# Optimization experiments

Measured on AMD Instinct MI355X. Metric: run time of the kernel, lower is better.

The kernel has to match this reference:

```python
import jax, jax.numpy as jnp
import numpy as np

B, S, HQ, HKV, D = 2, 2048, 32, 8, 128
ROPE_BASE = 10000.0
NEG_INF = -1e9


def setup_inputs() -> dict:
    key = jax.random.key(0)
    kq, kk, kv = jax.random.split(key, 3)
    q = jax.random.normal(kq, (B, S, HQ, D), dtype=jnp.float32)
    k = jax.random.normal(kk, (B, S, HKV, D), dtype=jnp.float32)
    v = jax.random.normal(kv, (B, S, HKV, D), dtype=jnp.float32)
    # Llama rotary tables: [S, D] with freqs duplicated across the two halves
    inv_freq = 1.0 / (ROPE_BASE ** (jnp.arange(0, D, 2, dtype=jnp.float32) / D))
    freqs = jnp.arange(S, dtype=jnp.float32)[:, None] * inv_freq[None, :]  # [S, D/2]
    emb = jnp.concatenate([freqs, freqs], axis=-1)  # [S, D]
    cos = jnp.cos(emb)
    sin = jnp.sin(emb)
    # causal additive mask [B, 1, S, S]: 0 on/below diagonal, -1e9 above
    causal = jnp.tril(jnp.ones((S, S), dtype=bool))
    attention_mask = jnp.where(causal, 0.0, NEG_INF).astype(jnp.float32)
    attention_mask = jnp.broadcast_to(attention_mask[None, None], (B, 1, S, S))
    return {
        "query_states": q,
        "key_states": k,
        "value_states": v,
        "cos": cos,
        "sin": sin,
        "attention_mask": attention_mask,
        "softmax_scale": float(1.0 / np.sqrt(D)),
    }


def _rotate_half(x):
    h = x.shape[-1] // 2
    return jnp.concatenate([-x[..., h:], x[..., :h]], axis=-1)


def _apply_rope(x, cos, sin):
    # x: [B, S, H, D]; cos/sin: [S, D] -> broadcast over batch and heads
    c = cos[None, :, None, :]
    s = sin[None, :, None, :]
    return x * c + _rotate_half(x) * s


def reference(query_states, key_states, value_states, cos, sin, attention_mask, softmax_scale):
    if attention_mask.ndim == 4 and attention_mask.shape[1] == 1:
        attention_mask = attention_mask[:, 0]  # [B, S, S]
    q = _apply_rope(query_states, cos, sin)          # [B, S, HQ, D]
    k = _apply_rope(key_states, cos, sin)            # [B, S, HKV, D]
    v = value_states                                  # [B, S, HKV, D]
    groups = q.shape[2] // k.shape[2]
    k = jnp.repeat(k, groups, axis=2)                 # [B, S, HQ, D]
    v = jnp.repeat(v, groups, axis=2)
    scores = jnp.einsum("bqhd,bkhd->bhqk", q, k) * softmax_scale
    scores = scores + attention_mask[:, None, :, :]   # broadcast over heads
    probs = jax.nn.softmax(scores, axis=-1)
    out = jnp.einsum("bhqk,bkhd->bqhd", probs, v)     # [B, S, HQ, D]
    return out
```

## Files before the change

kernel.cpp:

```cpp
#include <hip/hip_runtime.h>
#include <stdint.h>

typedef unsigned short u16;
typedef unsigned int   u32;
typedef short bf16x8 __attribute__((ext_vector_type(8)));
typedef u16   u16x8  __attribute__((ext_vector_type(8)));
typedef u16   u16x4  __attribute__((ext_vector_type(4)));
typedef float f32x4  __attribute__((ext_vector_type(4)));

#define B_   2
#define S_   2048
#define HQ_  32
#define HKV_ 8
#define D_   128
#define SCALE 0.08838834764831845f

#define KR_ELEMS (B_*HKV_*S_*D_)

#define KT_BLOCKS ((B_*S_*HKV_*16) / 256)
#define VT_BLOCKS (B_*HKV_*(S_/64))

#define SWZ(x) ((x) ^ (((x) >> 3) & 0x70))

__device__ __forceinline__ float b2f(u16 x) { return __uint_as_float(((u32)x) << 16); }
__device__ __forceinline__ u16 f2b(float f) {
  u32 u = __float_as_uint(f);
  return (u16)((u + 0x7FFFu + ((u >> 16) & 1u)) >> 16);
}
__device__ __forceinline__ bool is_f32(const void* cs) {
  return ((const u32*)cs)[0] == 0x3F800000u;
}

__device__ __forceinline__ void gload16(const u16* g, u16* l) {
  __builtin_amdgcn_global_load_lds(
      (const __attribute__((address_space(1))) u32*)g,
      (__attribute__((address_space(3))) u32*)l, 16, 0, 0);
}

__global__ __launch_bounds__(256) void rope_pre(
    const void* __restrict__ kin, const void* __restrict__ vin,
    const void* __restrict__ cs, const void* __restrict__ sn, u16* __restrict__ ws)
{
  const bool f32 = is_f32(cs);
  const int bx = blockIdx.x;
  const int t  = threadIdx.x;
  __shared__ u16 tile[64 * 136];

  if (bx < KT_BLOCKS) {
    int tid = bx*256 + t;
    int j4 = tid & 15;
    int s  = (tid >> 4) & (S_ - 1);
    int h  = (tid >> 15) & (HKV_ - 1);
    int b  = tid >> 18;
    int gi = ((b*S_ + s)*HKV_ + h)*D_ + 4*j4;
    int ci = s*D_ + 4*j4;
    float xa[4], xb[4], c[4], si[4];
    if (f32) {
      const float* kf = (const float*)kin;
      f32x4 a0 = *(const f32x4*)(kf + gi);
      f32x4 b0 = *(const f32x4*)(kf + gi + 64);
      f32x4 c0 = *(const f32x4*)((const float*)cs + ci);
      f32x4 s0 = *(const f32x4*)((const float*)sn + ci);
#pragma unroll
      for (int e = 0; e < 4; ++e) { xa[e]=a0[e]; xb[e]=b0[e]; c[e]=c0[e]; si[e]=s0[e]; }
    } else {
      const u16* kb16 = (const u16*)kin;
      u16x4 a0 = *(const u16x4*)(kb16 + gi);
      u16x4 b0 = *(const u16x4*)(kb16 + gi + 64);
      u16x4 c0 = *(const u16x4*)((const u16*)cs + ci);
      u16x4 s0 = *(const u16x4*)((const u16*)sn + ci);
#pragma unroll
      for (int e = 0; e < 4; ++e) { xa[e]=b2f(a0[e]); xb[e]=b2f(b0[e]); c[e]=b2f(c0[e]); si[e]=b2f(s0[e]); }
    }
    u16 o0[4], o1[4];
#pragma unroll
    for (int e = 0; e < 4; ++e) {
      o0[e] = f2b(xa[e]*c[e] - xb[e]*si[e]);
      o1[e] = f2b(xb[e]*c[e] + xa[e]*si[e]);
    }
    int oi = ((b*HKV_ + h)*S_ + s)*D_ + 4*j4;
    *(u16x4*)(ws + oi)      = *(u16x4*)o0;
    *(u16x4*)(ws + oi + 64) = *(u16x4*)o1;
  } else {
    int vb = bx - KT_BLOCKS;
    int sb = vb & 31;
    int h  = (vb >> 5) & (HKV_ - 1);
    int b  = vb >> 8;
    int s0 = sb * 64;
#pragma unroll
    for (int it = 0; it < 8; ++it) {
      int task = it*256 + t;
      int c4 = task & 31;
      int r  = task >> 5;
      int gi = ((b*S_ + s0 + r)*HKV_ + h)*D_ + 4*c4;
      u16 e[4];
      if (f32) {
        f32x4 a = *(const f32x4*)((const float*)vin + gi);
#pragma unroll
        for (int j = 0; j < 4; ++j) e[j] = f2b(a[j]);
      } else {
        u16x4 a = *(const u16x4*)((const u16*)vin + gi);
#pragma unroll
        for (int j = 0; j < 4; ++j) e[j] = a[j];
      }
      *(u16x4*)&tile[r*136 + 4*c4] = *(u16x4*)e;
    }
    __syncthreads();
    u32* vtd = (u32*)(ws + KR_ELEMS) + (b*HKV_ + h)*D_*(S_/2);
#pragma unroll
    for (int it = 0; it < 16; ++it) {
      int task = it*256 + t;
      int sp = task & 31, d = task >> 5;
      u32 lo = tile[(2*sp)*136 + d];
      u32 hi = tile[(2*sp + 1)*136 + d];
      vtd[d*(S_/2) + s0/2 + sp] = lo | (hi << 16);
    }
  }
}

__device__ __forceinline__ void stage_tile(const u16* __restrict__ Kr,
                                           const u16* __restrict__ Vt,
                                           u16* lds, int bufbyte, int n0, int t) {
#pragma unroll
  for (int it = 0; it < 2; ++it) {
    int a = (t + it*256) * 16;
    int l = SWZ(a);
    gload16(Kr + (n0 + ((l >> 6) & 31))*D_ + (l >> 11)*32 + ((l >> 4) & 3)*8,
            (u16*)((char*)lds + bufbyte + a));
  }
#pragma unroll
  for (int it = 0; it < 2; ++it) {
    int a = (t + it*256) * 16;
    int l = SWZ(a);
    gload16(Vt + (l >> 6)*S_ + n0 + ((l >> 4) & 3)*8,
            (u16*)((char*)lds + bufbyte + 8192 + a));
  }
}

__global__ __launch_bounds__(256, 4) void flash_attn(
    const void* __restrict__ qg, const void* __restrict__ cs, const void* __restrict__ sn,
    const u16* __restrict__ ws, float* __restrict__ out)
{
  __shared__ __attribute__((aligned(16))) u16 lds[18944];

  const bool f32 = is_f32(cs);
  const int t = threadIdx.x;
  const int lane = t & 63, w = t >> 6;
  const int lq = lane & 15, quad = lane >> 4;

  int bx = blockIdx.x;
  int g = bx & 7, ii = bx >> 3;
  int combo = g*2 + (ii >> 6);
  int b = combo >> 3, kvh = combo & 7;
  int rr = ii & 63;
  int h   = kvh*4 + (rr & 3);
  int qbp = rr >> 2;

  const u16* Kr = ws + (b*HKV_ + kvh)*S_*D_;
  const u16* Vt = ws + KR_ELEMS + (b*HKV_ + kvh)*D_*S_;

  for (int half = 0; half < 2; ++half) {
    int qb = half ? (31 - qbp) : qbp;
    int q0 = qb * 64;
    if (half) __syncthreads();

#pragma unroll
    for (int it = 0; it < 2; ++it) {
      int tp = it*256 + t;
      int row = tp >> 3, j = tp & 7;
      int qbase = ((b*S_ + q0 + row)*HQ_ + h)*D_ + 8*j;
      int cbase = (q0 + row)*D_ + 8*j;
      float a[8], bb[8], cc[8], ssv[8];
      if (f32) {
        const float* qf32 = (const float*)qg;
        f32x4 a0 = *(const f32x4*)(qf32 + qbase);
        f32x4 a1 = *(const f32x4*)(qf32 + qbase + 4);
        f32x4 b0 = *(const f32x4*)(qf32 + qbase + 64);
        f32x4 b1 = *(const f32x4*)(qf32 + qbase + 68);
        f32x4 c0 = *(const f32x4*)((const float*)cs + cbase);
        f32x4 c1 = *(const f32x4*)((const float*)cs + cbase + 4);
        f32x4 s0 = *(const f32x4*)((const float*)sn + cbase);
        f32x4 s1 = *(const f32x4*)((const float*)sn + cbase + 4);
#pragma unroll
        for (int e = 0; e < 4; ++e) {
          a[e] = a0[e];  a[4+e] = a1[e];  bb[e] = b0[e]; bb[4+e] = b1[e];
          cc[e] = c0[e]; cc[4+e] = c1[e]; ssv[e] = s0[e]; ssv[4+e] = s1[e];
        }
      } else {
        const u16* qb16 = (const u16*)qg;
        u16x8 xa = *(const u16x8*)(qb16 + qbase);
        u16x8 xb = *(const u16x8*)(qb16 + qbase + 64);
        u16x8 cv = *(const u16x8*)((const u16*)cs + cbase);
        u16x8 sv = *(const u16x8*)((const u16*)sn + cbase);
#pragma unroll
        for (int e = 0; e < 8; ++e) {
          a[e] = b2f(xa[e]); bb[e] = b2f(xb[e]);
          cc[e] = b2f(cv[e]); ssv[e] = b2f(sv[e]);
        }
      }
      u16 o0[8], o1[8];
#pragma unroll
      for (int e = 0; e < 8; ++e) {
        o0[e] = f2b(a[e]*cc[e] - bb[e]*ssv[e]);
        o1[e] = f2b(bb[e]*cc[e] + a[e]*ssv[e]);
      }
      int A0 = (j >> 2)*4096 + row*64 + (j & 3)*16;
      int A1 = A0 + 8192;
      *(u16x8*)((char*)lds + SWZ(A0)) = *(u16x8*)o0;
      *(u16x8*)((char*)lds + SWZ(A1)) = *(u16x8*)o1;
    }
    __syncthreads();
    bf16x8 qf[4];
    const int R = w*16 + lq;
#pragma unroll
    for (int c = 0; c < 4; ++c) {
      int L = c*4096 + R*64 + quad*16;
      qf[c] = *(const bf16x8*)((const char*)lds + SWZ(L));
    }
    asm volatile("s_waitcnt lgkmcnt(0)" ::: "memory");
    __syncthreads();

    f32x4 o[8];
#pragma unroll
    for (int dt = 0; dt < 8; ++dt) o[dt] = (f32x4){0.f, 0.f, 0.f, 0.f};
    float m_i = -1e30f, l_i = 0.f;
    const int qrow = q0 + w*16 + lq;
    const int nkb = 2*qb + 2;

    stage_tile(Kr, Vt, lds, 0, 0, t);

    for (int kb = 0; kb < nkb; ++kb) {
      const int cur = kb & 1;
      asm volatile("" ::: "memory");
      __builtin_amdgcn_s_barrier();
      asm volatile("" ::: "memory");
      if (kb + 1 < nkb) {
        stage_tile(Kr, Vt, lds, (cur ^ 1)*16384, (kb + 1)*32, t);
        asm volatile("s_waitcnt vmcnt(4)" ::: "memory");
      } else {
        asm volatile("s_waitcnt vmcnt(0)" ::: "memory");
      }
      __builtin_amdgcn_s_barrier();
      asm volatile("" ::: "memory");

      const int n0 = kb * 32;
      const char* kbase = (const char*)lds + cur*16384;
      const char* vbase = kbase + 8192;

      f32x4 sc0 = {0,0,0,0}, sc1 = {0,0,0,0};
#pragma unroll
      for (int c = 0; c < 4; ++c) {
        int L0 = c*2048 + lq*64 + quad*16;
        int L1 = L0 + 1024;
        bf16x8 k0 = *(const bf16x8*)(kbase + SWZ(L0));
        bf16x8 k1 = *(const bf16x8*)(kbase + SWZ(L1));
        sc0 = __builtin_amdgcn_mfma_f32_16x16x32_bf16(k0, qf[c], sc0, 0, 0, 0);
        sc1 = __builtin_amdgcn_mfma_f32_16x16x32_bf16(k1, qf[c], sc1, 0, 0, 0);
      }

      const int kk = n0 + quad*4;
      float s0[4], s1[4];
#pragma unroll
      for (int r = 0; r < 4; ++r) {
        s0[r] = (kk + r      <= qrow) ? sc0[r]*SCALE : -1e30f;
        s1[r] = (kk + 16 + r <= qrow) ? sc1[r]*SCALE : -1e30f;
      }
      float mx = fmaxf(fmaxf(fmaxf(s0[0], s0[1]), fmaxf(s0[2], s0[3])),
                       fmaxf(fmaxf(s1[0], s1[1]), fmaxf(s1[2], s1[3])));
      mx = fmaxf(mx, __shfl_xor(mx, 16));
      mx = fmaxf(mx, __shfl_xor(mx, 32));
      if (!__all(mx - m_i <= 8.0f)) {
        float mn = fmaxf(m_i, mx);
        float al = __expf(m_i - mn);
        l_i *= al;
#pragma unroll
        for (int dt = 0; dt < 8; ++dt) {
#pragma unroll
          for (int r = 0; r < 4; ++r) o[dt][r] *= al;
        }
        m_i = mn;
      }
      float p0[4], p1[4];
      float rs = 0.f;
#pragma unroll
      for (int r = 0; r < 4; ++r) {
        p0[r] = __expf(s0[r] - m_i);
        p1[r] = __expf(s1[r] - m_i);
        rs += p0[r] + p1[r];
      }
      rs += __shfl_xor(rs, 16);
      rs += __shfl_xor(rs, 32);
      l_i += rs;

      u16* pw = &lds[16384 + w*640];
      u16 pk0[4], pk1[4];
#pragma unroll
      for (int r = 0; r < 4; ++r) { pk0[r] = f2b(p0[r]); pk1[r] = f2b(p1[r]); }
      *(uint64_t*)&pw[lq*40 + quad*4]      = *(uint64_t*)pk0;
      *(uint64_t*)&pw[lq*40 + 16 + quad*4] = *(uint64_t*)pk1;
      asm volatile("s_waitcnt lgkmcnt(0)" ::: "memory");
      bf16x8 pf = *(const bf16x8*)&pw[lq*40 + quad*8];

#pragma unroll
      for (int dt = 0; dt < 8; ++dt) {
        int Lv = (dt*16 + lq)*64 + quad*16;
        bf16x8 vf = *(const bf16x8*)(vbase + SWZ(Lv));
        o[dt] = __builtin_amdgcn_mfma_f32_16x16x32_bf16(vf, pf, o[dt], 0, 0, 0);
      }
    }

    float inv = 1.0f / l_i;
    float* op = out + ((b*S_ + qrow)*HQ_ + h)*D_ + quad*4;
#pragma unroll
    for (int dt = 0; dt < 8; ++dt) {
      f32x4 v = { o[dt][0]*inv, o[dt][1]*inv, o[dt][2]*inv, o[dt][3]*inv };
      *(f32x4*)(op + dt*16) = v;
    }
  }
}

extern "C" void kernel_launch(void* const* d_in, const int* in_sizes, int n_in,
                              void* d_out, int out_size, void* d_ws, size_t ws_size,
                              hipStream_t stream) {
  const void* q  = d_in[0];
  const void* k  = d_in[1];
  const void* v  = d_in[2];
  const void* cs = d_in[3];
  const void* sn = d_in[4];
  u16*   ws  = (u16*)d_ws;
  float* out = (float*)d_out;

  rope_pre<<<KT_BLOCKS + VT_BLOCKS, 256, 0, stream>>>(k, v, cs, sn, ws);
  flash_attn<<<B_*HQ_*(S_/128), 256, 0, stream>>>(q, cs, sn, ws, out);
}
```

Before: 283.2 us.

## Fold scale into Q rope, use exp2, permlane reductions, and register P transpose

Folds softmax scale times log2(e) into the Q RoPE so the inner loop can use exp2 without a per-score multiply, and applies the causal mask only on diagonal blocks. Replaces the shuffle-based row max/sum reductions with permlane16/32 swaps. Builds the bf16 P operand in registers with v_cvt_pk_bf16 and permlane swaps instead of a round trip through LDS, which shrinks LDS use. It also precomputes swizzled LDS and global addresses and raises the rescale threshold, at the cost of relying on gfx950-specific builtins and on correct permlane lane mapping.

```diff
diff --git a/kernel.cpp b/kernel.cpp
--- a/kernel.cpp
+++ b/kernel.cpp
@@ -13,7 +13,7 @@
 #define HQ_  32
 #define HKV_ 8
 #define D_   128
-#define SCALE 0.08838834764831845f
+#define SC2  0.1275174457530659f
 
 #define KR_ELEMS (B_*HKV_*S_*D_)
 
@@ -29,6 +29,42 @@
 }
 __device__ __forceinline__ bool is_f32(const void* cs) {
   return ((const u32*)cs)[0] == 0x3F800000u;
+}
+
+#if __has_builtin(__builtin_amdgcn_exp2f)
+#define EXP2(x) __builtin_amdgcn_exp2f(x)
+#else
+#define EXP2(x) exp2f(x)
+#endif
+
+__device__ __forceinline__ void pl32(u32& a, u32& b) {
+  auto r = __builtin_amdgcn_permlane32_swap((int)a, (int)b, false, false);
+  a = (u32)r[0]; b = (u32)r[1];
+}
+__device__ __forceinline__ void pl16(u32& a, u32& b) {
+  auto r = __builtin_amdgcn_permlane16_swap((int)a, (int)b, false, false);
+  a = (u32)r[0]; b = (u32)r[1];
+}
+__device__ __forceinline__ float qredmax(float x) {
+  u32 a = __float_as_uint(x), b = a;
+  pl16(a, b);
+  float m = fmaxf(__uint_as_float(a), __uint_as_float(b));
+  u32 c = __float_as_uint(m), d = c;
+  pl32(c, d);
+  return fmaxf(__uint_as_float(c), __uint_as_float(d));
+}
+__device__ __forceinline__ float qredsum(float x) {
+  u32 a = __float_as_uint(x), b = a;
+  pl16(a, b);
+  float m = __uint_as_float(a) + __uint_as_float(b);
+  u32 c = __float_as_uint(m), d = c;
+  pl32(c, d);
+  return __uint_as_float(c) + __uint_as_float(d);
+}
+__device__ __forceinline__ u32 cvtpk(float lo, float hi) {
+  u32 r;
+  asm("v_cvt_pk_bf16_f32 %0, %1, %2" : "=v"(r) : "v"(lo), "v"(hi));
+  return r;
 }
 
 __device__ __forceinline__ void gload16(const u16* g, u16* l) {
@@ -118,35 +154,19 @@
   }
 }
 
-__device__ __forceinline__ void stage_tile(const u16* __restrict__ Kr,
-                                           const u16* __restrict__ Vt,
-                                           u16* lds, int bufbyte, int n0, int t) {
-#pragma unroll
-  for (int it = 0; it < 2; ++it) {
-    int a = (t + it*256) * 16;
-    int l = SWZ(a);
-    gload16(Kr + (n0 + ((l >> 6) & 31))*D_ + (l >> 11)*32 + ((l >> 4) & 3)*8,
-            (u16*)((char*)lds + bufbyte + a));
-  }
-#pragma unroll
-  for (int it = 0; it < 2; ++it) {
-    int a = (t + it*256) * 16;
-    int l = SWZ(a);
-    gload16(Vt + (l >> 6)*S_ + n0 + ((l >> 4) & 3)*8,
-            (u16*)((char*)lds + bufbyte + 8192 + a));
-  }
-}
-
 __global__ __launch_bounds__(256, 4) void flash_attn(
     const void* __restrict__ qg, const void* __restrict__ cs, const void* __restrict__ sn,
     const u16* __restrict__ ws, float* __restrict__ out)
 {
-  __shared__ __attribute__((aligned(16))) u16 lds[18944];
+  __shared__ __attribute__((aligned(16))) u16 lds[16384];
+  char* ldsc = (char*)lds;
 
   const bool f32 = is_f32(cs);
   const int t = threadIdx.x;
   const int lane = t & 63, w = t >> 6;
   const int lq = lane & 15, quad = lane >> 4;
+
+  const int kq = (lq*64 + quad*16) ^ (((lq >> 1) & 7) << 4);
 
   int bx = blockIdx.x;
   int g = bx & 7, ii = bx >> 3;
@@ -158,6 +178,20 @@
 
   const u16* Kr = ws + (b*HKV_ + kvh)*S_*D_;
   const u16* Vt = ws + KR_ELEMS + (b*HKV_ + kvh)*D_*S_;
+
+  const int aK0 = t*16, aK1 = t*16 + 4096;
+  const int lA0 = SWZ(aK0), lA1 = SWZ(aK1);
+  const u16* kg0 = Kr + ((lA0 >> 6) & 31)*D_ + (lA0 >> 11)*32 + ((lA0 >> 4) & 3)*8;
+  const u16* kg1 = Kr + ((lA1 >> 6) & 31)*D_ + (lA1 >> 11)*32 + ((lA1 >> 4) & 3)*8;
+  const u16* vg0 = Vt + (lA0 >> 6)*S_ + ((lA0 >> 4) & 3)*8;
+  const u16* vg1 = Vt + (lA1 >> 6)*S_ + ((lA1 >> 4) & 3)*8;
+
+#define STAGE(bufbyte, n0v) do {                                   \
+    gload16(kg0 + (n0v)*D_, (u16*)(ldsc + (bufbyte) + aK0));       \
+    gload16(kg1 + (n0v)*D_, (u16*)(ldsc + (bufbyte) + aK1));       \
+    gload16(vg0 + (n0v),    (u16*)(ldsc + (bufbyte) + 8192 + aK0));\
+    gload16(vg1 + (n0v),    (u16*)(ldsc + (bufbyte) + 8192 + aK1));\
+  } while (0)
 
   for (int half = 0; half < 2; ++half) {
     int qb = half ? (31 - qbp) : qbp;
@@ -201,22 +235,20 @@
       u16 o0[8], o1[8];
 #pragma unroll
       for (int e = 0; e < 8; ++e) {
-        o0[e] = f2b(a[e]*cc[e] - bb[e]*ssv[e]);
-        o1[e] = f2b(bb[e]*cc[e] + a[e]*ssv[e]);
+        float C2 = cc[e]*SC2, S2 = ssv[e]*SC2;
+        o0[e] = f2b(a[e]*C2 - bb[e]*S2);
+        o1[e] = f2b(bb[e]*C2 + a[e]*S2);
       }
       int A0 = (j >> 2)*4096 + row*64 + (j & 3)*16;
       int A1 = A0 + 8192;
-      *(u16x8*)((char*)lds + SWZ(A0)) = *(u16x8*)o0;
-      *(u16x8*)((char*)lds + SWZ(A1)) = *(u16x8*)o1;
+      *(u16x8*)(ldsc + SWZ(A0)) = *(u16x8*)o0;
+      *(u16x8*)(ldsc + SWZ(A1)) = *(u16x8*)o1;
     }
     __syncthreads();
     bf16x8 qf[4];
-    const int R = w*16 + lq;
-#pragma unroll
-    for (int c = 0; c < 4; ++c) {
-      int L = c*4096 + R*64 + quad*16;
-      qf[c] = *(const bf16x8*)((const char*)lds + SWZ(L));
-    }
+#pragma unroll
+    for (int c = 0; c < 4; ++c)
+      qf[c] = *(const bf16x8*)(ldsc + c*4096 + w*1024 + kq);
     asm volatile("s_waitcnt lgkmcnt(0)" ::: "memory");
     __syncthreads();
 
@@ -227,7 +259,7 @@
     const int qrow = q0 + w*16 + lq;
     const int nkb = 2*qb + 2;
 
-    stage_tile(Kr, Vt, lds, 0, 0, t);
+    STAGE(0, 0);
 
     for (int kb = 0; kb < nkb; ++kb) {
       const int cur = kb & 1;
@@ -235,7 +267,7 @@
       __builtin_amdgcn_s_barrier();
       asm volatile("" ::: "memory");
       if (kb + 1 < nkb) {
-        stage_tile(Kr, Vt, lds, (cur ^ 1)*16384, (kb + 1)*32, t);
+        STAGE((cur ^ 1) << 14, (kb + 1)*32);
         asm volatile("s_waitcnt vmcnt(4)" ::: "memory");
       } else {
         asm volatile("s_waitcnt vmcnt(0)" ::: "memory");
@@ -244,34 +276,34 @@
       asm volatile("" ::: "memory");
 
       const int n0 = kb * 32;
-      const char* kbase = (const char*)lds + cur*16384;
-      const char* vbase = kbase + 8192;
+      const char* tb = ldsc + (cur << 14) + kq;
 
       f32x4 sc0 = {0,0,0,0}, sc1 = {0,0,0,0};
 #pragma unroll
       for (int c = 0; c < 4; ++c) {
-        int L0 = c*2048 + lq*64 + quad*16;
-        int L1 = L0 + 1024;
-        bf16x8 k0 = *(const bf16x8*)(kbase + SWZ(L0));
-        bf16x8 k1 = *(const bf16x8*)(kbase + SWZ(L1));
+        bf16x8 k0 = *(const bf16x8*)(tb + c*2048);
+        bf16x8 k1 = *(const bf16x8*)(tb + c*2048 + 1024);
         sc0 = __builtin_amdgcn_mfma_f32_16x16x32_bf16(k0, qf[c], sc0, 0, 0, 0);
         sc1 = __builtin_amdgcn_mfma_f32_16x16x32_bf16(k1, qf[c], sc1, 0, 0, 0);
       }
 
-      const int kk = n0 + quad*4;
       float s0[4], s1[4];
 #pragma unroll
-      for (int r = 0; r < 4; ++r) {
-        s0[r] = (kk + r      <= qrow) ? sc0[r]*SCALE : -1e30f;
-        s1[r] = (kk + 16 + r <= qrow) ? sc1[r]*SCALE : -1e30f;
+      for (int r = 0; r < 4; ++r) { s0[r] = sc0[r]; s1[r] = sc1[r]; }
+      if (kb >= 2*qb) {
+        const int kk = n0 + quad*4;
+#pragma unroll
+        for (int r = 0; r < 4; ++r) {
+          if (kk + r      > qrow) s0[r] = -1e30f;
+          if (kk + 16 + r > qrow) s1[r] = -1e30f;
+        }
       }
       float mx = fmaxf(fmaxf(fmaxf(s0[0], s0[1]), fmaxf(s0[2], s0[3])),
                        fmaxf(fmaxf(s1[0], s1[1]), fmaxf(s1[2], s1[3])));
-      mx = fmaxf(mx, __shfl_xor(mx, 16));
-      mx = fmaxf(mx, __shfl_xor(mx, 32));
-      if (!__all(mx - m_i <= 8.0f)) {
+      mx = qredmax(mx);
+      if (!__all(mx - m_i <= 11.5f)) {
         float mn = fmaxf(m_i, mx);
-        float al = __expf(m_i - mn);
+        float al = EXP2(m_i - mn);
         l_i *= al;
 #pragma unroll
         for (int dt = 0; dt < 8; ++dt) {
@@ -284,27 +316,23 @@
       float rs = 0.f;
 #pragma unroll
       for (int r = 0; r < 4; ++r) {
-        p0[r] = __expf(s0[r] - m_i);
-        p1[r] = __expf(s1[r] - m_i);
+        p0[r] = EXP2(s0[r] - m_i);
+        p1[r] = EXP2(s1[r] - m_i);
         rs += p0[r] + p1[r];
       }
-      rs += __shfl_xor(rs, 16);
-      rs += __shfl_xor(rs, 32);
-      l_i += rs;
-
-      u16* pw = &lds[16384 + w*640];
-      u16 pk0[4], pk1[4];
-#pragma unroll
-      for (int r = 0; r < 4; ++r) { pk0[r] = f2b(p0[r]); pk1[r] = f2b(p1[r]); }
-      *(uint64_t*)&pw[lq*40 + quad*4]      = *(uint64_t*)pk0;
-      *(uint64_t*)&pw[lq*40 + 16 + quad*4] = *(uint64_t*)pk1;
-      asm volatile("s_waitcnt lgkmcnt(0)" ::: "memory");
-      bf16x8 pf = *(const bf16x8*)&pw[lq*40 + quad*8];
+      l_i += qredsum(rs);
+
+      u32 Y0 = cvtpk(p0[0], p0[1]), Y1 = cvtpk(p0[2], p0[3]);
+      u32 Z0 = cvtpk(p1[0], p1[1]), Z1 = cvtpk(p1[2], p1[3]);
+      pl32(Y0, Z0); pl16(Y0, Z0);
+      pl32(Y1, Z1); pl16(Y1, Z1);
+      union { u32 wd[4]; bf16x8 v; } pu;
+      pu.wd[0] = Y0; pu.wd[1] = Y1; pu.wd[2] = Z0; pu.wd[3] = Z1;
+      bf16x8 pf = pu.v;
 
 #pragma unroll
       for (int dt = 0; dt < 8; ++dt) {
-        int Lv = (dt*16 + lq)*64 + quad*16;
-        bf16x8 vf = *(const bf16x8*)(vbase + SWZ(Lv));
+        bf16x8 vf = *(const bf16x8*)(tb + 8192 + dt*1024);
         o[dt] = __builtin_amdgcn_mfma_f32_16x16x32_bf16(vf, pf, o[dt], 0, 0, 0);
       }
     }
@@ -317,6 +345,7 @@
       *(f32x4*)(op + dt*16) = v;
     }
   }
+#undef STAGE
 }
 
 extern "C" void kernel_launch(void* const* d_in, const int* in_sizes, int n_in,
```

Result: faster. 255.0 us (-9.9%).
